# Kernel optimization log

Measured on AMD Instinct MI355X. Metric: run time of the kernel, lower is better.

The kernel has to match this reference:

```python
import jax, jax.numpy as jnp
import numpy as np

N = 100000   # nodes
E = 3200000  # edges (avg degree 32)
F = 10       # input features
H = 20       # hidden dim
G = 512      # graphs in batch
L = 2        # labels


def xavier(key, shape):
    fan_in, fan_out = shape[0], shape[1]
    a = jnp.sqrt(6.0 / (fan_in + fan_out))
    return jax.random.uniform(key, shape, jnp.float32, -a, a)


def setup_inputs() -> dict:
    key = jax.random.key(0)
    ks = jax.random.split(key, 12)
    x = jax.random.normal(ks[0], (N, F), jnp.float32)
    edge_index = jax.random.randint(ks[1], (2, E), 0, N, jnp.int64)
    batch = jnp.sort(jax.random.randint(ks[2], (N,), 0, G, jnp.int64))
    return {
        "x": x,
        "edge_index": edge_index,
        "batch": batch,
        # layer 1: F -> H
        "W_rel1": xavier(ks[3], (F, H)), "b1": jnp.zeros((H,), jnp.float32),
        "W_root1": xavier(ks[4], (F, H)),
        # layer 2: H -> H
        "W_rel2": xavier(ks[5], (H, H)), "b2": jnp.zeros((H,), jnp.float32),
        "W_root2": xavier(ks[6], (H, H)),
        # layer 3: H -> H
        "W_rel3": xavier(ks[7], (H, H)), "b3": jnp.zeros((H,), jnp.float32),
        "W_root3": xavier(ks[8], (H, H)),
        # readout linear: 2H -> L
        "W_lin": xavier(ks[9], (2 * H, L)), "b_lin": jnp.zeros((L,), jnp.float32),
    }


def _graph_conv(x, src, dst, W_rel, b, W_root):
    # PyG GraphConv: out = lin_rel(sum_{j->i} x_j) + lin_root(x_i)
    agg = jax.ops.segment_sum(x[src], dst, num_segments=N)  # [N, d_in]
    return agg @ W_rel + b + x @ W_root


def reference(x, edge_index, batch, W_rel1, b1, W_root1, W_rel2, b2, W_root2,
              W_rel3, b3, W_root3, W_lin, b_lin):
    src, dst = edge_index[0], edge_index[1]
    h = jax.nn.relu(_graph_conv(x, src, dst, W_rel1, b1, W_root1))
    h = jax.nn.relu(_graph_conv(h, src, dst, W_rel2, b2, W_root2))
    h = jax.nn.relu(_graph_conv(h, src, dst, W_rel3, b3, W_root3))  # [N, H]
    # global max / mean pool over graphs
    maxp = jax.ops.segment_max(h, batch, num_segments=G)            # [G, H]
    sump = jax.ops.segment_sum(h, batch, num_segments=G)            # [G, H]
    counts = jax.ops.segment_sum(jnp.ones((h.shape[0], 1), h.dtype), batch,
                                 num_segments=G)                    # [G, 1]
    nonempty = counts > 0
    maxp = jnp.where(nonempty, maxp, 0.0)
    meanp = sump / jnp.maximum(counts, 1.0)
    pooled = jnp.concatenate([maxp, meanp], axis=-1)                # [G, 2H]
    return pooled @ W_lin + b_lin
```

## Files before the change

### kernel.cpp

```cpp
#include <hip/hip_runtime.h>
#include <hip/hip_bf16.h>

#define NN 100000
#define FF 10
#define HH 20
#define GG 512
#define LL 2

#define NB 500
#define BNODES 200
#define CAP 7168
#define HB 100
#define SCAP 3712
#define TILE 4096
#define SRC_BITS 17
#define SRC_MASK 0x1FFFFu

__device__ inline unsigned short f2bf(float f) {
  unsigned u = __float_as_uint(f);
  unsigned r = u + 0x7FFFu + ((u >> 16) & 1u);
  return (unsigned short)(r >> 16);
}
__device__ inline float bflo(unsigned u) { return __uint_as_float(u << 16); }
__device__ inline float bfhi(unsigned u) { return __uint_as_float(u & 0xFFFF0000u); }

struct __align__(4) u4a { unsigned x, y, z, w; };
struct __align__(4) u2a { unsigned x, y; };

__global__ __launch_bounds__(256) void cast_init_kernel(
    const float* __restrict__ x, unsigned short* __restrict__ xb,
    float* __restrict__ sump, int* __restrict__ maxp, float* __restrict__ cnt,
    int* __restrict__ cursor, int n) {
  int i = blockIdx.x * 256 + threadIdx.x;
  if (i < n) xb[i] = f2bf(__builtin_nontemporal_load(x + i));
  if (i < GG * HH) {
    sump[i] = 0.0f;
    maxp[i] = 0;
  }
  if (i < GG) cnt[i] = 0.0f;
  if (i < NB) cursor[i] = 0;
}

__global__ __launch_bounds__(512) void multisplit_kernel(
    const int* __restrict__ src, const int* __restrict__ dst,
    int* __restrict__ cursor, unsigned int* __restrict__ pay, int E) {
  __shared__ int lhist[NB];
  __shared__ int lofs[NB];
  __shared__ int gbase[NB];
  __shared__ int lcur[NB];
  __shared__ unsigned int sord[TILE];
  __shared__ unsigned short sdbk[TILE];
  __shared__ int ss[512];
  int t = threadIdx.x;
  if (t < NB) lhist[t] = 0;
  __syncthreads();

  int base = blockIdx.x * TILE;
  int count = E - base;
  if (count > TILE) count = TILE;

  for (int i = t; i < count; i += 512)
    atomicAdd(&lhist[dst[base + i] / BNODES], 1);
  __syncthreads();

  int own = (t < NB) ? lhist[t] : 0;
  ss[t] = own;
  __syncthreads();
  for (int off = 1; off < 512; off <<= 1) {
    int a0 = (t >= off) ? ss[t - off] : 0;
    __syncthreads();
    ss[t] += a0;
    __syncthreads();
  }
  if (t < NB) {
    lofs[t] = ss[t] - own;
    int bo = own ? atomicAdd(&cursor[t], own) : 0;
    if (bo > CAP - own) bo = CAP - own;
    gbase[t] = t * CAP + bo;
    lcur[t] = 0;
  }
  __syncthreads();

  for (int i = t; i < count; i += 512) {
    int e = base + i;
    int d = __builtin_nontemporal_load(dst + e);
    int s = __builtin_nontemporal_load(src + e);
    int bk = d / BNODES;
    int ld = d - bk * BNODES;
    int r = atomicAdd(&lcur[bk], 1);
    int slot = lofs[bk] + r;
    sord[slot] = ((unsigned)ld << SRC_BITS) | (unsigned)s;
    sdbk[slot] = (unsigned short)bk;
  }
  __syncthreads();

  for (int i = t; i < count; i += 512) {
    int bk = sdbk[i];
    pay[gbase[bk] + (i - lofs[bk])] = sord[i];
  }
}

__global__ __launch_bounds__(256) void bucket_csr_kernel(
    const unsigned int* __restrict__ pay, const int* __restrict__ cursor,
    int* __restrict__ srt, int* __restrict__ rofs, int* __restrict__ rend) {
  __shared__ int lhist[BNODES];
  __shared__ int lofs[BNODES];
  __shared__ int lcur[BNODES];
  __shared__ int ss[256];
  int b = blockIdx.x;
  int t = threadIdx.x;
  int k0 = b * CAP;
  int ecnt = cursor[b];
  if (ecnt > CAP) ecnt = CAP;

  if (t < BNODES) lhist[t] = 0;
  __syncthreads();
  for (int k = t; k < ecnt; k += 256)
    atomicAdd(&lhist[pay[k0 + k] >> SRC_BITS], 1);
  __syncthreads();

  int own = (t < BNODES) ? lhist[t] : 0;
  ss[t] = own;
  __syncthreads();
  for (int off = 1; off < 256; off <<= 1) {
    int a0 = (t >= off) ? ss[t - off] : 0;
    __syncthreads();
    ss[t] += a0;
    __syncthreads();
  }
  if (t < BNODES) {
    int ex = ss[t] - own;
    lofs[t] = ex;
    lcur[t] = 0;
    rofs[b * BNODES + t] = k0 + ex;
    rend[b * BNODES + t] = k0 + ex + own;
  }
  __syncthreads();

  for (int k = t; k < ecnt; k += 256) {
    unsigned p = pay[k0 + k];
    int ld = p >> SRC_BITS;
    int r = atomicAdd(&lcur[ld], 1);
    srt[k0 + lofs[ld] + r] = (int)(p & SRC_MASK);
  }
}

template<int DIN>
__global__ __launch_bounds__(512, 8) void bucket_layer_kernel(
    const unsigned short* __restrict__ hin, const int* __restrict__ srt,
    const int* __restrict__ rofs, const int* __restrict__ rend,
    const float* __restrict__ Wrel, const float* __restrict__ bias,
    const float* __restrict__ Wroot, unsigned short* __restrict__ hout) {
  constexpr int AST = (DIN == 10) ? 11 : 21;
  constexpr int NP = (DIN == 10) ? 2 : 3;
  __shared__ int sSrc[SCAP];
  __shared__ float acc[HB * AST];
  __shared__ unsigned short roots[HB * DIN];
  __shared__ float sWrel[DIN * HH];
  __shared__ float sWroot[DIN * HH];
  __shared__ float sb[HH];
  __shared__ int sRofs[HB];
  __shared__ int sRend[HB];
  __shared__ int sSeg0, sSegLen;
  int b2 = blockIdx.x;
  int t = threadIdx.x;
  int nbase = b2 * HB;

  for (int i = t; i < DIN * HH; i += 512) {
    sWrel[i] = Wrel[i];
    sWroot[i] = Wroot[i];
  }
  if (t < HH) sb[t] = bias[t];
  if (t < HB) {
    sRofs[t] = rofs[nbase + t];
    sRend[t] = rend[nbase + t];
  }
  if (t == 0) {
    int s0 = rofs[nbase];
    int sl = rend[nbase + HB - 1] - s0;
    sSeg0 = s0;
    sSegLen = sl < SCAP ? sl : SCAP;
  }
  {
    const unsigned* rs = (const unsigned*)(hin + (size_t)nbase * DIN);
    unsigned* rd = (unsigned*)roots;
    for (int i = t; i < HB * DIN / 2; i += 512) rd[i] = rs[i];
  }
  __syncthreads();

  int seg0 = sSeg0, seglen = sSegLen;
  for (int i = t; i < seglen; i += 512) sSrc[i] = srt[seg0 + i];
  __syncthreads();

  if (t < HB * NP) {
    int ln = t / NP;
    int p = t - ln * NP;
    int k0 = sRofs[ln] - seg0;
    int k1 = sRend[ln] - seg0;
    if (k1 > seglen) k1 = seglen;
    if (p * 8 + 8 <= DIN) {
      const unsigned short* bp = hin + p * 8;
      float a0 = 0, a1 = 0, a2 = 0, a3 = 0, a4 = 0, a5 = 0, a6 = 0, a7 = 0;
      for (int k = k0; k < k1; k++) {
        u4a u = *(const u4a*)(bp + (size_t)sSrc[k] * DIN);
        a0 += bflo(u.x); a1 += bfhi(u.x);
        a2 += bflo(u.y); a3 += bfhi(u.y);
        a4 += bflo(u.z); a5 += bfhi(u.z);
        a6 += bflo(u.w); a7 += bfhi(u.w);
      }
      float* ap = acc + ln * AST + p * 8;
      ap[0] = a0; ap[1] = a1; ap[2] = a2; ap[3] = a3;
      ap[4] = a4; ap[5] = a5; ap[6] = a6; ap[7] = a7;
    } else if (DIN == 10) {
      const unsigned short* bp = hin + 8;
      float a0 = 0, a1 = 0;
      for (int k = k0; k < k1; k++) {
        unsigned u = *(const unsigned*)(bp + (size_t)sSrc[k] * DIN);
        a0 += bflo(u); a1 += bfhi(u);
      }
      float* ap = acc + ln * AST + 8;
      ap[0] = a0; ap[1] = a1;
    } else {
      const unsigned short* bp = hin + 16;
      float a0 = 0, a1 = 0, a2 = 0, a3 = 0;
      for (int k = k0; k < k1; k++) {
        u2a u = *(const u2a*)(bp + (size_t)sSrc[k] * DIN);
        a0 += bflo(u.x); a1 += bfhi(u.x);
        a2 += bflo(u.y); a3 += bfhi(u.y);
      }
      float* ap = acc + ln * AST + 16;
      ap[0] = a0; ap[1] = a1; ap[2] = a2; ap[3] = a3;
    }
  }
  __syncthreads();

  for (int idx = t; idx < HB * HH; idx += 512) {
    int ln = idx / HH;
    int j = idx - ln * HH;
    const float* a = acc + ln * AST;
    const unsigned short* r = roots + ln * DIN;
    float v = sb[j];
#pragma unroll
    for (int f = 0; f < DIN; f++) {
      v += a[f] * sWrel[f * HH + j];
      v += bflo((unsigned)r[f]) * sWroot[f * HH + j];
    }
    hout[(size_t)nbase * HH + idx] = f2bf(fmaxf(v, 0.0f));
  }
}

__global__ __launch_bounds__(512, 8) void bucket_layer_pool_kernel(
    const unsigned short* __restrict__ hin, const int* __restrict__ srt,
    const int* __restrict__ rofs, const int* __restrict__ rend,
    const float* __restrict__ Wrel, const float* __restrict__ bias,
    const float* __restrict__ Wroot, const int* __restrict__ batch,
    float* __restrict__ sump, int* __restrict__ maxp,
    float* __restrict__ cnt) {
  constexpr int DIN = 20;
  constexpr int AST = 21;
  constexpr int NP = 3;
  __shared__ int sSrc[SCAP];
  __shared__ float acc[HB * AST];
  __shared__ unsigned short roots[HB * DIN];
  __shared__ int sBatch[HB];
  __shared__ float sWrel[DIN * HH];
  __shared__ float sWroot[DIN * HH];
  __shared__ float sb[HH];
  __shared__ int sRofs[HB];
  __shared__ int sRend[HB];
  __shared__ int sSeg0, sSegLen;
  int b2 = blockIdx.x;
  int t = threadIdx.x;
  int nbase = b2 * HB;

  for (int i = t; i < DIN * HH; i += 512) {
    sWrel[i] = Wrel[i];
    sWroot[i] = Wroot[i];
  }
  if (t < HH) sb[t] = bias[t];
  if (t < HB) {
    sRofs[t] = rofs[nbase + t];
    sRend[t] = rend[nbase + t];
    sBatch[t] = batch[nbase + t];
  }
  if (t == 0) {
    int s0 = rofs[nbase];
    int sl = rend[nbase + HB - 1] - s0;
    sSeg0 = s0;
    sSegLen = sl < SCAP ? sl : SCAP;
  }
  {
    const unsigned* rs = (const unsigned*)(hin + (size_t)nbase * DIN);
    unsigned* rd = (unsigned*)roots;
    for (int i = t; i < HB * DIN / 2; i += 512) rd[i] = rs[i];
  }
  __syncthreads();

  int seg0 = sSeg0, seglen = sSegLen;
  for (int i = t; i < seglen; i += 512) sSrc[i] = srt[seg0 + i];
  __syncthreads();

  if (t < HB * NP) {
    int ln = t / NP;
    int p = t - ln * NP;
    int k0 = sRofs[ln] - seg0;
    int k1 = sRend[ln] - seg0;
    if (k1 > seglen) k1 = seglen;
    if (p < 2) {
      const unsigned short* bp = hin + p * 8;
      float a0 = 0, a1 = 0, a2 = 0, a3 = 0, a4 = 0, a5 = 0, a6 = 0, a7 = 0;
      for (int k = k0; k < k1; k++) {
        u4a u = *(const u4a*)(bp + (size_t)sSrc[k] * DIN);
        a0 += bflo(u.x); a1 += bfhi(u.x);
        a2 += bflo(u.y); a3 += bfhi(u.y);
        a4 += bflo(u.z); a5 += bfhi(u.z);
        a6 += bflo(u.w); a7 += bfhi(u.w);
      }
      float* ap = acc + ln * AST + p * 8;
      ap[0] = a0; ap[1] = a1; ap[2] = a2; ap[3] = a3;
      ap[4] = a4; ap[5] = a5; ap[6] = a6; ap[7] = a7;
    } else {
      const unsigned short* bp = hin + 16;
      float a0 = 0, a1 = 0, a2 = 0, a3 = 0;
      for (int k = k0; k < k1; k++) {
        u2a u = *(const u2a*)(bp + (size_t)sSrc[k] * DIN);
        a0 += bflo(u.x); a1 += bfhi(u.x);
        a2 += bflo(u.y); a3 += bfhi(u.y);
      }
      float* ap = acc + ln * AST + 16;
      ap[0] = a0; ap[1] = a1; ap[2] = a2; ap[3] = a3;
    }
  }
  __syncthreads();

  float vreg[4];
#pragma unroll
  for (int u = 0; u < 4; u++) {
    int idx = t + u * 512;
    if (idx < HB * HH) {
      int ln = idx / HH;
      int j = idx - ln * HH;
      const float* a = acc + ln * AST;
      const unsigned short* r = roots + ln * DIN;
      float v = sb[j];
#pragma unroll
      for (int f = 0; f < DIN; f++) {
        v += a[f] * sWrel[f * HH + j];
        v += bflo((unsigned)r[f]) * sWroot[f * HH + j];
      }
      vreg[u] = fmaxf(v, 0.0f);
    }
  }
  __syncthreads();
#pragma unroll
  for (int u = 0; u < 4; u++) {
    int idx = t + u * 512;
    if (idx < HB * HH) {
      int ln = idx / HH;
      int j = idx - ln * HH;
      acc[ln * AST + j] = vreg[u];
    }
  }
  __syncthreads();

  int g0 = sBatch[0];
  int g1 = sBatch[HB - 1];
  int ngr = g1 - g0 + 1;
  for (int it = t; it < ngr * HH; it += 512) {
    int gi = it / HH;
    int j = it - gi * HH;
    int g = g0 + gi;
    float s = 0.0f, m = 0.0f;
    int c = 0;
    for (int ln = 0; ln < HB; ln++) {
      if (sBatch[ln] == g) {
        float v = acc[ln * AST + j];
        s += v;
        m = fmaxf(m, v);
        c++;
      }
    }
    if (c) {
      atomicAdd(&sump[g * HH + j], s);
      atomicMax(&maxp[g * HH + j], __float_as_int(m));
      if (j == 0) atomicAdd(&cnt[g], (float)c);
    }
  }
}

__global__ __launch_bounds__(256) void readout_kernel(
    const float* __restrict__ sump, const int* __restrict__ maxp,
    const float* __restrict__ cnt, const float* __restrict__ Wlin,
    const float* __restrict__ blin, float* __restrict__ out) {
  int idx = blockIdx.x * 256 + threadIdx.x;
  if (idx >= GG * LL) return;
  int g = idx / LL;
  int l = idx - g * LL;
  float c = cnt[g];
  float inv = 1.0f / fmaxf(c, 1.0f);
  float acc = blin[l];
#pragma unroll
  for (int j = 0; j < HH; j++) {
    float mx = __int_as_float(maxp[g * HH + j]);
    float mean = sump[g * HH + j] * inv;
    acc += mx * Wlin[j * LL + l];
    acc += mean * Wlin[(HH + j) * LL + l];
  }
  out[idx] = acc;
}

extern "C" void kernel_launch(void* const* d_in, const int* in_sizes, int n_in,
                              void* d_out, int out_size, void* d_ws,
                              size_t ws_size, hipStream_t stream) {
  const float* x = (const float*)d_in[0];
  const int* edge_index = (const int*)d_in[1];
  const int* batch = (const int*)d_in[2];
  const float* W_rel1 = (const float*)d_in[3];
  const float* b1 = (const float*)d_in[4];
  const float* W_root1 = (const float*)d_in[5];
  const float* W_rel2 = (const float*)d_in[6];
  const float* b2 = (const float*)d_in[7];
  const float* W_root2 = (const float*)d_in[8];
  const float* W_rel3 = (const float*)d_in[9];
  const float* b3 = (const float*)d_in[10];
  const float* W_root3 = (const float*)d_in[11];
  const float* W_lin = (const float*)d_in[12];
  const float* b_lin = (const float*)d_in[13];
  float* out = (float*)d_out;

  const int E = in_sizes[1] / 2;
  const int n_nodes = in_sizes[0] / FF;
  const int* src = edge_index;
  const int* dst = edge_index + E;

  unsigned int* pay = (unsigned int*)d_ws;
  int* srt = (int*)(pay + (size_t)NB * CAP);
  int* rofs = srt + (size_t)NB * CAP;
  int* rend = rofs + NN;
  int* cursor = rend + NN;
  float* sump = (float*)(cursor + 512);
  int* maxp = (int*)(sump + GG * HH);
  float* cnt = (float*)(maxp + GG * HH);
  unsigned short* xb = (unsigned short*)(cnt + 512);
  unsigned short* h1 = xb + (size_t)NN * FF;
  unsigned short* h2 = h1 + (size_t)NN * HH;

  const int edge_tiles = (E + TILE - 1) / TILE;

  cast_init_kernel<<<(n_nodes * FF + 255) / 256, 256, 0, stream>>>(
      x, xb, sump, maxp, cnt, cursor, n_nodes * FF);

  multisplit_kernel<<<edge_tiles, 512, 0, stream>>>(src, dst, cursor, pay, E);
  bucket_csr_kernel<<<NB, 256, 0, stream>>>(pay, cursor, srt, rofs, rend);

  bucket_layer_kernel<FF><<<NB * 2, 512, 0, stream>>>(
      xb, srt, rofs, rend, W_rel1, b1, W_root1, h1);
  bucket_layer_kernel<HH><<<NB * 2, 512, 0, stream>>>(
      h1, srt, rofs, rend, W_rel2, b2, W_root2, h2);
  bucket_layer_pool_kernel<<<NB * 2, 512, 0, stream>>>(
      h2, srt, rofs, rend, W_rel3, b3, W_root3, batch, sump, maxp, cnt);

  readout_kernel<<<(GG * LL + 255) / 256, 256, 0, stream>>>(
      sump, maxp, cnt, W_lin, b_lin, out);
}
```

Measured before the change: 299.4 us.

## Split node features into aligned 16-wide and tail arrays for vector gathers

Node feature storage is split into two planar arrays: an aligned main block (8 or 16 bf16 values per node) and a small tail array (2 or 4 values). Row gathers can then use naturally aligned 16-byte and 8-byte loads instead of loads from rows with a 20- or 40-byte stride. The gather loops are also unrolled by two so each thread has two independent loads in flight. The tail gather is moved to a separate group of threads (256+), which adds work to the root-load and output-write paths and changes how threads are assigned to nodes.

```diff
diff --git a/kernel.cpp b/kernel.cpp
--- a/kernel.cpp
+++ b/kernel.cpp
@@ -16,6 +16,7 @@
 #define SRC_BITS 17
 #define SRC_MASK 0x1FFFFu
 
+
 __device__ inline unsigned short f2bf(float f) {
   unsigned u = __float_as_uint(f);
   unsigned r = u + 0x7FFFu + ((u >> 16) & 1u);
@@ -24,15 +25,22 @@
 __device__ inline float bflo(unsigned u) { return __uint_as_float(u << 16); }
 __device__ inline float bfhi(unsigned u) { return __uint_as_float(u & 0xFFFF0000u); }
 
-struct __align__(4) u4a { unsigned x, y, z, w; };
-struct __align__(4) u2a { unsigned x, y; };
-
 __global__ __launch_bounds__(256) void cast_init_kernel(
-    const float* __restrict__ x, unsigned short* __restrict__ xb,
+    const float* __restrict__ x, unsigned short* __restrict__ xA,
+    unsigned short* __restrict__ xB,
     float* __restrict__ sump, int* __restrict__ maxp, float* __restrict__ cnt,
-    int* __restrict__ cursor, int n) {
+    int* __restrict__ cursor, int n_nodes) {
   int i = blockIdx.x * 256 + threadIdx.x;
-  if (i < n) xb[i] = f2bf(__builtin_nontemporal_load(x + i));
+  if (i < n_nodes * 8) {
+    int node = i >> 3;
+    int f = i & 7;
+    xA[i] = f2bf(__builtin_nontemporal_load(x + (size_t)node * FF + f));
+  }
+  if (i < n_nodes * 2) {
+    int node = i >> 1;
+    int f = i & 1;
+    xB[i] = f2bf(__builtin_nontemporal_load(x + (size_t)node * FF + 8 + f));
+  }
   if (i < GG * HH) {
     sump[i] = 0.0f;
     maxp[i] = 0;
@@ -147,15 +155,18 @@
 
 template<int DIN>
 __global__ __launch_bounds__(512, 8) void bucket_layer_kernel(
-    const unsigned short* __restrict__ hin, const int* __restrict__ srt,
+    const unsigned short* __restrict__ hA, const unsigned short* __restrict__ hB,
+    const int* __restrict__ srt,
     const int* __restrict__ rofs, const int* __restrict__ rend,
     const float* __restrict__ Wrel, const float* __restrict__ bias,
-    const float* __restrict__ Wroot, unsigned short* __restrict__ hout) {
-  constexpr int AST = (DIN == 10) ? 11 : 21;
-  constexpr int NP = (DIN == 10) ? 2 : 3;
+    const float* __restrict__ Wroot,
+    unsigned short* __restrict__ oA, unsigned short* __restrict__ oB) {
+  constexpr int AST = DIN + 1;
+  constexpr int AW = (DIN == 10) ? 8 : 16;
+  constexpr int ALN = AW / 8;
   __shared__ int sSrc[SCAP];
   __shared__ float acc[HB * AST];
-  __shared__ unsigned short roots[HB * DIN];
+  __shared__ unsigned roots32[HB * DIN / 2];
   __shared__ float sWrel[DIN * HH];
   __shared__ float sWroot[DIN * HH];
   __shared__ float sb[HH];
@@ -182,9 +193,18 @@
     sSegLen = sl < SCAP ? sl : SCAP;
   }
   {
-    const unsigned* rs = (const unsigned*)(hin + (size_t)nbase * DIN);
-    unsigned* rd = (unsigned*)roots;
-    for (int i = t; i < HB * DIN / 2; i += 512) rd[i] = rs[i];
+    const unsigned* rsA = (const unsigned*)(hA + (size_t)nbase * AW);
+    for (int i = t; i < HB * (AW / 2); i += 512) {
+      int ln = i / (AW / 2);
+      int p = i - ln * (AW / 2);
+      roots32[ln * (DIN / 2) + p] = rsA[i];
+    }
+    const unsigned* rsB = (const unsigned*)(hB + (size_t)nbase * (DIN - AW));
+    for (int i = t; i < HB * ((DIN - AW) / 2); i += 512) {
+      int ln = i / ((DIN - AW) / 2);
+      int p = i - ln * ((DIN - AW) / 2);
+      roots32[ln * (DIN / 2) + AW / 2 + p] = rsB[i];
+    }
   }
   __syncthreads();
 
@@ -192,44 +212,77 @@
   for (int i = t; i < seglen; i += 512) sSrc[i] = srt[seg0 + i];
   __syncthreads();
 
-  if (t < HB * NP) {
-    int ln = t / NP;
-    int p = t - ln * NP;
+  if (t < HB * ALN) {
+    int ln = t / ALN;
+    int c = t - ln * ALN;
     int k0 = sRofs[ln] - seg0;
     int k1 = sRend[ln] - seg0;
     if (k1 > seglen) k1 = seglen;
-    if (p * 8 + 8 <= DIN) {
-      const unsigned short* bp = hin + p * 8;
-      float a0 = 0, a1 = 0, a2 = 0, a3 = 0, a4 = 0, a5 = 0, a6 = 0, a7 = 0;
-      for (int k = k0; k < k1; k++) {
-        u4a u = *(const u4a*)(bp + (size_t)sSrc[k] * DIN);
+    const unsigned short* bp = hA + c * 8;
+    float a0 = 0, a1 = 0, a2 = 0, a3 = 0, a4 = 0, a5 = 0, a6 = 0, a7 = 0;
+    int k = k0;
+    for (; k + 1 < k1; k += 2) {
+      uint4 u = *(const uint4*)(bp + (size_t)sSrc[k] * AW);
+      uint4 v = *(const uint4*)(bp + (size_t)sSrc[k + 1] * AW);
+      a0 += bflo(u.x); a1 += bfhi(u.x);
+      a2 += bflo(u.y); a3 += bfhi(u.y);
+      a4 += bflo(u.z); a5 += bfhi(u.z);
+      a6 += bflo(u.w); a7 += bfhi(u.w);
+      a0 += bflo(v.x); a1 += bfhi(v.x);
+      a2 += bflo(v.y); a3 += bfhi(v.y);
+      a4 += bflo(v.z); a5 += bfhi(v.z);
+      a6 += bflo(v.w); a7 += bfhi(v.w);
+    }
+    if (k < k1) {
+      uint4 u = *(const uint4*)(bp + (size_t)sSrc[k] * AW);
+      a0 += bflo(u.x); a1 += bfhi(u.x);
+      a2 += bflo(u.y); a3 += bfhi(u.y);
+      a4 += bflo(u.z); a5 += bfhi(u.z);
+      a6 += bflo(u.w); a7 += bfhi(u.w);
+    }
+    float* ap = acc + ln * AST + c * 8;
+    ap[0] = a0; ap[1] = a1; ap[2] = a2; ap[3] = a3;
+    ap[4] = a4; ap[5] = a5; ap[6] = a6; ap[7] = a7;
+  }
+
+  if (t >= 256 && t < 256 + HB) {
+    int ln = t - 256;
+    int k0 = sRofs[ln] - seg0;
+    int k1 = sRend[ln] - seg0;
+    if (k1 > seglen) k1 = seglen;
+    if (DIN == 20) {
+      float a0 = 0, a1 = 0, a2 = 0, a3 = 0;
+      int k = k0;
+      for (; k + 1 < k1; k += 2) {
+        uint2 u = *(const uint2*)(hB + (size_t)sSrc[k] * 4);
+        uint2 v = *(const uint2*)(hB + (size_t)sSrc[k + 1] * 4);
         a0 += bflo(u.x); a1 += bfhi(u.x);
         a2 += bflo(u.y); a3 += bfhi(u.y);
-        a4 += bflo(u.z); a5 += bfhi(u.z);
-        a6 += bflo(u.w); a7 += bfhi(u.w);
+        a0 += bflo(v.x); a1 += bfhi(v.x);
+        a2 += bflo(v.y); a3 += bfhi(v.y);
       }
-      float* ap = acc + ln * AST + p * 8;
-      ap[0] = a0; ap[1] = a1; ap[2] = a2; ap[3] = a3;
-      ap[4] = a4; ap[5] = a5; ap[6] = a6; ap[7] = a7;
-    } else if (DIN == 10) {
-      const unsigned short* bp = hin + 8;
-      float a0 = 0, a1 = 0;
-      for (int k = k0; k < k1; k++) {
-        unsigned u = *(const unsigned*)(bp + (size_t)sSrc[k] * DIN);
-        a0 += bflo(u); a1 += bfhi(u);
-      }
-      float* ap = acc + ln * AST + 8;
-      ap[0] = a0; ap[1] = a1;
-    } else {
-      const unsigned short* bp = hin + 16;
-      float a0 = 0, a1 = 0, a2 = 0, a3 = 0;
-      for (int k = k0; k < k1; k++) {
-        u2a u = *(const u2a*)(bp + (size_t)sSrc[k] * DIN);
+      if (k < k1) {
+        uint2 u = *(const uint2*)(hB + (size_t)sSrc[k] * 4);
         a0 += bflo(u.x); a1 += bfhi(u.x);
         a2 += bflo(u.y); a3 += bfhi(u.y);
       }
       float* ap = acc + ln * AST + 16;
       ap[0] = a0; ap[1] = a1; ap[2] = a2; ap[3] = a3;
+    } else {
+      float a0 = 0, a1 = 0;
+      int k = k0;
+      for (; k + 1 < k1; k += 2) {
+        unsigned u = *(const unsigned*)(hB + (size_t)sSrc[k] * 2);
+        unsigned v = *(const unsigned*)(hB + (size_t)sSrc[k + 1] * 2);
+        a0 += bflo(u) + bflo(v);
+        a1 += bfhi(u) + bfhi(v);
+      }
+      if (k < k1) {
+        unsigned u = *(const unsigned*)(hB + (size_t)sSrc[k] * 2);
+        a0 += bflo(u); a1 += bfhi(u);
+      }
+      float* ap = acc + ln * AST + 8;
+      ap[0] = a0; ap[1] = a1;
     }
   }
   __syncthreads();
@@ -238,19 +291,22 @@
     int ln = idx / HH;
     int j = idx - ln * HH;
     const float* a = acc + ln * AST;
-    const unsigned short* r = roots + ln * DIN;
+    const unsigned short* r = (const unsigned short*)(roots32 + ln * (DIN / 2));
     float v = sb[j];
 #pragma unroll
     for (int f = 0; f < DIN; f++) {
       v += a[f] * sWrel[f * HH + j];
       v += bflo((unsigned)r[f]) * sWroot[f * HH + j];
     }
-    hout[(size_t)nbase * HH + idx] = f2bf(fmaxf(v, 0.0f));
+    unsigned short hv = f2bf(fmaxf(v, 0.0f));
+    if (j < 16) oA[(size_t)(nbase + ln) * 16 + j] = hv;
+    else        oB[(size_t)(nbase + ln) * 4 + (j - 16)] = hv;
   }
 }
 
 __global__ __launch_bounds__(512, 8) void bucket_layer_pool_kernel(
-    const unsigned short* __restrict__ hin, const int* __restrict__ srt,
+    const unsigned short* __restrict__ hA, const unsigned short* __restrict__ hB,
+    const int* __restrict__ srt,
     const int* __restrict__ rofs, const int* __restrict__ rend,
     const float* __restrict__ Wrel, const float* __restrict__ bias,
     const float* __restrict__ Wroot, const int* __restrict__ batch,
@@ -258,10 +314,9 @@
     float* __restrict__ cnt) {
   constexpr int DIN = 20;
   constexpr int AST = 21;
-  constexpr int NP = 3;
   __shared__ int sSrc[SCAP];
   __shared__ float acc[HB * AST];
-  __shared__ unsigned short roots[HB * DIN];
+  __shared__ unsigned roots32[HB * 10];
   __shared__ int sBatch[HB];
   __shared__ float sWrel[DIN * HH];
   __shared__ float sWroot[DIN * HH];
@@ -290,9 +345,18 @@
     sSegLen = sl < SCAP ? sl : SCAP;
   }
   {
-    const unsigned* rs = (const unsigned*)(hin + (size_t)nbase * DIN);
-    unsigned* rd = (unsigned*)roots;
-    for (int i = t; i < HB * DIN / 2; i += 512) rd[i] = rs[i];
+    const unsigned* rsA = (const unsigned*)(hA + (size_t)nbase * 16);
+    for (int i = t; i < HB * 8; i += 512) {
+      int ln = i / 8;
+      int p = i - ln * 8;
+      roots32[ln * 10 + p] = rsA[i];
+    }
+    const unsigned* rsB = (const unsigned*)(hB + (size_t)nbase * 4);
+    for (int i = t; i < HB * 2; i += 512) {
+      int ln = i / 2;
+      int p = i - ln * 2;
+      roots32[ln * 10 + 8 + p] = rsB[i];
+    }
   }
   __syncthreads();
 
@@ -300,36 +364,61 @@
   for (int i = t; i < seglen; i += 512) sSrc[i] = srt[seg0 + i];
   __syncthreads();
 
-  if (t < HB * NP) {
-    int ln = t / NP;
-    int p = t - ln * NP;
+  if (t < HB * 2) {
+    int ln = t / 2;
+    int c = t - ln * 2;
     int k0 = sRofs[ln] - seg0;
     int k1 = sRend[ln] - seg0;
     if (k1 > seglen) k1 = seglen;
-    if (p < 2) {
-      const unsigned short* bp = hin + p * 8;
-      float a0 = 0, a1 = 0, a2 = 0, a3 = 0, a4 = 0, a5 = 0, a6 = 0, a7 = 0;
-      for (int k = k0; k < k1; k++) {
-        u4a u = *(const u4a*)(bp + (size_t)sSrc[k] * DIN);
-        a0 += bflo(u.x); a1 += bfhi(u.x);
-        a2 += bflo(u.y); a3 += bfhi(u.y);
-        a4 += bflo(u.z); a5 += bfhi(u.z);
-        a6 += bflo(u.w); a7 += bfhi(u.w);
-      }
-      float* ap = acc + ln * AST + p * 8;
-      ap[0] = a0; ap[1] = a1; ap[2] = a2; ap[3] = a3;
-      ap[4] = a4; ap[5] = a5; ap[6] = a6; ap[7] = a7;
-    } else {
-      const unsigned short* bp = hin + 16;
-      float a0 = 0, a1 = 0, a2 = 0, a3 = 0;
-      for (int k = k0; k < k1; k++) {
-        u2a u = *(const u2a*)(bp + (size_t)sSrc[k] * DIN);
-        a0 += bflo(u.x); a1 += bfhi(u.x);
-        a2 += bflo(u.y); a3 += bfhi(u.y);
-      }
-      float* ap = acc + ln * AST + 16;
-      ap[0] = a0; ap[1] = a1; ap[2] = a2; ap[3] = a3;
-    }
+    const unsigned short* bp = hA + c * 8;
+    float a0 = 0, a1 = 0, a2 = 0, a3 = 0, a4 = 0, a5 = 0, a6 = 0, a7 = 0;
+    int k = k0;
+    for (; k + 1 < k1; k += 2) {
+      uint4 u = *(const uint4*)(bp + (size_t)sSrc[k] * 16);
+      uint4 v = *(const uint4*)(bp + (size_t)sSrc[k + 1] * 16);
+      a0 += bflo(u.x); a1 += bfhi(u.x);
+      a2 += bflo(u.y); a3 += bfhi(u.y);
+      a4 += bflo(u.z); a5 += bfhi(u.z);
+      a6 += bflo(u.w); a7 += bfhi(u.w);
+      a0 += bflo(v.x); a1 += bfhi(v.x);
+      a2 += bflo(v.y); a3 += bfhi(v.y);
+      a4 += bflo(v.z); a5 += bfhi(v.z);
+      a6 += bflo(v.w); a7 += bfhi(v.w);
+    }
+    if (k < k1) {
+      uint4 u = *(const uint4*)(bp + (size_t)sSrc[k] * 16);
+      a0 += bflo(u.x); a1 += bfhi(u.x);
+      a2 += bflo(u.y); a3 += bfhi(u.y);
+      a4 += bflo(u.z); a5 += bfhi(u.z);
+      a6 += bflo(u.w); a7 += bfhi(u.w);
+    }
+    float* ap = acc + ln * AST + c * 8;
+    ap[0] = a0; ap[1] = a1; ap[2] = a2; ap[3] = a3;
+    ap[4] = a4; ap[5] = a5; ap[6] = a6; ap[7] = a7;
+  }
+
+  if (t >= 256 && t < 256 + HB) {
+    int ln = t - 256;
+    int k0 = sRofs[ln] - seg0;
+    int k1 = sRend[ln] - seg0;
+    if (k1 > seglen) k1 = seglen;
+    float a0 = 0, a1 = 0, a2 = 0, a3 = 0;
+    int k = k0;
+    for (; k + 1 < k1; k += 2) {
+      uint2 u = *(const uint2*)(hB + (size_t)sSrc[k] * 4);
+      uint2 v = *(const uint2*)(hB + (size_t)sSrc[k + 1] * 4);
+      a0 += bflo(u.x); a1 += bfhi(u.x);
+      a2 += bflo(u.y); a3 += bfhi(u.y);
+      a0 += bflo(v.x); a1 += bfhi(v.x);
+      a2 += bflo(v.y); a3 += bfhi(v.y);
+    }
+    if (k < k1) {
+      uint2 u = *(const uint2*)(hB + (size_t)sSrc[k] * 4);
+      a0 += bflo(u.x); a1 += bfhi(u.x);
+      a2 += bflo(u.y); a3 += bfhi(u.y);
+    }
+    float* ap = acc + ln * AST + 16;
+    ap[0] = a0; ap[1] = a1; ap[2] = a2; ap[3] = a3;
   }
   __syncthreads();
 
@@ -341,7 +430,7 @@
       int ln = idx / HH;
       int j = idx - ln * HH;
       const float* a = acc + ln * AST;
-      const unsigned short* r = roots + ln * DIN;
+      const unsigned short* r = (const unsigned short*)(roots32 + ln * 10);
       float v = sb[j];
 #pragma unroll
       for (int f = 0; f < DIN; f++) {
@@ -441,24 +530,27 @@
   float* sump = (float*)(cursor + 512);
   int* maxp = (int*)(sump + GG * HH);
   float* cnt = (float*)(maxp + GG * HH);
-  unsigned short* xb = (unsigned short*)(cnt + 512);
-  unsigned short* h1 = xb + (size_t)NN * FF;
-  unsigned short* h2 = h1 + (size_t)NN * HH;
+  unsigned short* xA = (unsigned short*)(cnt + 512);
+  unsigned short* xB = xA + (size_t)NN * 8;
+  unsigned short* h1A = xB + (size_t)NN * 2;
+  unsigned short* h1B = h1A + (size_t)NN * 16;
+  unsigned short* h2A = h1B + (size_t)NN * 4;
+  unsigned short* h2B = h2A + (size_t)NN * 16;
 
   const int edge_tiles = (E + TILE - 1) / TILE;
 
-  cast_init_kernel<<<(n_nodes * FF + 255) / 256, 256, 0, stream>>>(
-      x, xb, sump, maxp, cnt, cursor, n_nodes * FF);
+  cast_init_kernel<<<(n_nodes * 8 + 255) / 256, 256, 0, stream>>>(
+      x, xA, xB, sump, maxp, cnt, cursor, n_nodes);
 
   multisplit_kernel<<<edge_tiles, 512, 0, stream>>>(src, dst, cursor, pay, E);
   bucket_csr_kernel<<<NB, 256, 0, stream>>>(pay, cursor, srt, rofs, rend);
 
   bucket_layer_kernel<FF><<<NB * 2, 512, 0, stream>>>(
-      xb, srt, rofs, rend, W_rel1, b1, W_root1, h1);
+      xA, xB, srt, rofs, rend, W_rel1, b1, W_root1, h1A, h1B);
   bucket_layer_kernel<HH><<<NB * 2, 512, 0, stream>>>(
-      h1, srt, rofs, rend, W_rel2, b2, W_root2, h2);
+      h1A, h1B, srt, rofs, rend, W_rel2, b2, W_root2, h2A, h2B);
   bucket_layer_pool_kernel<<<NB * 2, 512, 0, stream>>>(
-      h2, srt, rofs, rend, W_rel3, b3, W_root3, batch, sump, maxp, cnt);
+      h2A, h2B, srt, rofs, rend, W_rel3, b3, W_root3, batch, sump, maxp, cnt);
 
   readout_kernel<<<(GG * LL + 255) / 256, 256, 0, stream>>>(
       sump, maxp, cnt, W_lin, b_lin, out);
```

After: 278.9 us. 1.07x faster.
